# Kernel tuning notes

Measured on AMD Instinct MI355X. Metric: run time of the kernel, lower is better.

## Reference

```python
import jax, jax.numpy as jnp
import numpy as np

N, L, CS, CZ, CH, H = 1, 768, 384, 128, 32, 12
EPS = 1e-5


def _layernorm(x, w, b):
    m = jnp.mean(x, axis=-1, keepdims=True)
    v = jnp.mean((x - m) ** 2, axis=-1, keepdims=True)
    return (x - m) * jax.lax.rsqrt(v + EPS) * w + b


def setup_inputs() -> dict:
    key = jax.random.key(0)
    ks = jax.random.split(key, 12)
    scale = 0.02
    return {
        "s": jax.random.normal(ks[0], (N, L, CS), jnp.float32),
        "z": jax.random.normal(ks[1], (N, L, L, CZ), jnp.float32),
        "ln_s_w": jnp.ones((CS,), jnp.float32),
        "ln_s_b": jnp.zeros((CS,), jnp.float32),
        "ln_z_w": jnp.ones((CZ,), jnp.float32),
        "ln_z_b": jnp.zeros((CZ,), jnp.float32),
        "w_z": jax.random.normal(ks[2], (H, CZ), jnp.float32) * scale,   # pair-bias proj (no bias)
        "w_q": jax.random.normal(ks[3], (H * CH, CS), jnp.float32) * scale,
        "w_k": jax.random.normal(ks[4], (H * CH, CS), jnp.float32) * scale,
        "w_v": jax.random.normal(ks[5], (H * CH, CS), jnp.float32) * scale,
        "w_g": jax.random.normal(ks[6], (H * CH, CS), jnp.float32) * scale,
        "b_g": jnp.zeros((H * CH,), jnp.float32),
        "w_o": jax.random.normal(ks[7], (CS, H * CH), jnp.float32) * scale,
        "b_o": jnp.zeros((CS,), jnp.float32),
    }


def reference(s, z, ln_s_w, ln_s_b, ln_z_w, ln_z_b, w_z, w_q, w_k, w_v, w_g, b_g, w_o, b_o):
    s_n = _layernorm(s, ln_s_w, ln_s_b)            # [N,L,CS]
    z_n = _layernorm(z, ln_z_w, ln_z_b)            # [N,L,L,CZ]
    # pair bias: Linear(c_z -> H, bias=False), then permute to [N,H,L,L]
    bias = jnp.einsum("nijc,hc->nhij", z_n, w_z)   # [N,H,L,L]
    # AF2-style gated MHA on s
    q = jnp.einsum("nlc,dc->nld", s_n, w_q).reshape(N, L, H, CH) * (CH ** -0.5)
    k = jnp.einsum("nlc,dc->nld", s_n, w_k).reshape(N, L, H, CH)
    v = jnp.einsum("nlc,dc->nld", s_n, w_v).reshape(N, L, H, CH)
    logits = jnp.einsum("nqhc,nkhc->nhqk", q, k) + bias
    a = jax.nn.softmax(logits, axis=-1)
    o = jnp.einsum("nhqk,nkhc->nqhc", a, v).reshape(N, L, H * CH)
    g = jax.nn.sigmoid(jnp.einsum("nlc,dc->nld", s_n, w_g) + b_g)
    o = o * g
    return jnp.einsum("nld,cd->nlc", o, w_o) + b_o  # [N,L,CS]
```

## Files before the change

kernel.cpp:

```cpp
#include <hip/hip_runtime.h>
#include <hip/hip_bf16.h>
#include <cstddef>

#define L_ 768
#define CS_ 384
#define CZ_ 128
#define CH_ 32
#define H_ 12
#define LL_ (L_*L_)
#define EPS_ 1e-5f

typedef float f4 __attribute__((ext_vector_type(4)));

__global__ void prep_kernel(const float* __restrict__ lnzw, const float* __restrict__ lnzb,
                            const float* __restrict__ wz,
                            float* __restrict__ ww, float* __restrict__ sumww,
                            float* __restrict__ bb) {
    int h = threadIdx.x;
    if (h < H_) {
        float sw = 0.f, sb = 0.f;
        for (int c = 0; c < CZ_; ++c) {
            float wv = lnzw[c] * wz[h*CZ_ + c];
            ww[h*CZ_ + c] = wv;
            sw += wv;
            sb += lnzb[c] * wz[h*CZ_ + c];
        }
        sumww[h] = sw;
        bb[h] = sb;
    }
}

__device__ __forceinline__ void bias_issue(const float* gbase, float* ldst, int c) {
    #pragma unroll
    for (int j = 0; j < 8; ++j)
        __builtin_amdgcn_global_load_lds(
            (const __attribute__((address_space(1))) unsigned int*)(gbase + c*32 + j*4),
            (__attribute__((address_space(3))) unsigned int*)(ldst + j*1024),
            16, 0, 0);
}

__global__ __launch_bounds__(256) void bias_kernel(const float* __restrict__ z,
        const float* __restrict__ ww, const float* __restrict__ sumww,
        const float* __restrict__ bb, float* __restrict__ bias) {
    __shared__ float zbuf[2*8192];
    __shared__ float lw[H_*CZ_];
    __shared__ float lsw[H_];
    __shared__ float lbb[H_];

    const int tid   = threadIdx.x;
    const int w     = tid >> 6;
    const int l     = tid & 63;
    const int rbase = blockIdx.x * 256;

    const float* gbase = z + (size_t)(rbase + w*64 + l)*CZ_;

    for (int i = tid; i < H_*CZ_; i += 256) lw[i] = ww[i];
    if (tid < H_) { lsw[tid] = sumww[tid]; lbb[tid] = bb[tid]; }

    float acc[H_];
    #pragma unroll
    for (int h = 0; h < H_; ++h) acc[h] = 0.f;
    float sum = 0.f, sum2 = 0.f;

    bias_issue(gbase, zbuf + w*256, 0);
    __syncthreads();

    int cur = 0;
    #pragma unroll 1
    for (int c0 = 0; c0 < 4; ++c0) {
        if (c0 < 3)
            bias_issue(gbase, zbuf + (cur^1)*8192 + w*256, c0+1);
        #pragma unroll
        for (int j = 0; j < 8; ++j) {
            f4 zv = *(const f4*)&zbuf[cur*8192 + j*1024 + tid*4];
            const int cbase = c0*32 + j*4;
            sum  += zv.x + zv.y + zv.z + zv.w;
            sum2 += zv.x*zv.x + zv.y*zv.y + zv.z*zv.z + zv.w*zv.w;
            #pragma unroll
            for (int h = 0; h < H_; ++h) {
                f4 wv = *(const f4*)&lw[h*CZ_ + cbase];
                acc[h] += zv.x*wv.x + zv.y*wv.y + zv.z*wv.z + zv.w*wv.w;
            }
        }
        __syncthreads();
        cur ^= 1;
    }

    float m = sum * (1.f/CZ_);
    float r = rsqrtf(sum2*(1.f/CZ_) - m*m + EPS_);
    #pragma unroll
    for (int h = 0; h < H_; ++h)
        zbuf[tid*17 + h] = r*(acc[h] - m*lsw[h]) + lbb[h];
    __syncthreads();
    #pragma unroll
    for (int it = 0; it < 3; ++it) {
        int idx = it*256 + tid;
        int h   = idx >> 6;
        int qd  = idx & 63;
        f4 o;
        o.x = zbuf[(qd*4 + 0)*17 + h];
        o.y = zbuf[(qd*4 + 1)*17 + h];
        o.z = zbuf[(qd*4 + 2)*17 + h];
        o.w = zbuf[(qd*4 + 3)*17 + h];
        *(f4*)(bias + (size_t)h*LL_ + rbase + qd*4) = o;
    }
}

__global__ void sln_kernel(const float* __restrict__ s, const float* __restrict__ w,
                           const float* __restrict__ b, float* __restrict__ sn) {
    int row = blockIdx.x;
    int lane = threadIdx.x;
    float x[6];
    float sum = 0.f, sum2 = 0.f;
    #pragma unroll
    for (int j = 0; j < 6; ++j) {
        x[j] = s[row*CS_ + lane + j*64];
        sum += x[j]; sum2 += x[j]*x[j];
    }
    #pragma unroll
    for (int off = 32; off; off >>= 1) {
        sum  += __shfl_xor(sum,  off);
        sum2 += __shfl_xor(sum2, off);
    }
    float m = sum * (1.f/CS_);
    float r = rsqrtf(sum2*(1.f/CS_) - m*m + EPS_);
    #pragma unroll
    for (int j = 0; j < 6; ++j) {
        int c = lane + j*64;
        sn[row*CS_ + c] = (x[j]-m)*r*w[c] + b[c];
    }
}

__global__ __launch_bounds__(256) void qkvg_kernel(const float* __restrict__ sn,
        const float* __restrict__ wq, const float* __restrict__ wk,
        const float* __restrict__ wv, const float* __restrict__ wg,
        const float* __restrict__ bg,
        float* __restrict__ qb, float* __restrict__ kb,
        float* __restrict__ vb, float* __restrict__ gb) {
    __shared__ float As[16][68];
    __shared__ float Bs[16][68];
    int m0 = blockIdx.x * 64;
    int n0 = blockIdx.y * 64;
    int sel = n0 / 384;
    const float* W = (sel==0) ? wq : (sel==1) ? wk : (sel==2) ? wv : wg;
    float* C       = (sel==0) ? qb : (sel==1) ? kb : (sel==2) ? vb : gb;
    int ncol0 = n0 - sel*384;

    int t  = threadIdx.x;
    int lr = t >> 2;
    int lc = (t & 3) * 4;
    int ty = t >> 4;
    int tx = t & 15;

    float acc[4][4] = {};
    for (int k0 = 0; k0 < CS_; k0 += 16) {
        float4 av = *(const float4*)(sn + (size_t)(m0 + lr)*CS_ + k0 + lc);
        float4 bv = *(const float4*)(W  + (size_t)(ncol0 + lr)*CS_ + k0 + lc);
        As[lc+0][lr] = av.x; As[lc+1][lr] = av.y; As[lc+2][lr] = av.z; As[lc+3][lr] = av.w;
        Bs[lc+0][lr] = bv.x; Bs[lc+1][lr] = bv.y; Bs[lc+2][lr] = bv.z; Bs[lc+3][lr] = bv.w;
        __syncthreads();
        #pragma unroll
        for (int kk = 0; kk < 16; ++kk) {
            float4 a4 = *(const float4*)&As[kk][ty*4];
            float4 b4 = *(const float4*)&Bs[kk][tx*4];
            float a[4] = {a4.x,a4.y,a4.z,a4.w};
            float bb_[4] = {b4.x,b4.y,b4.z,b4.w};
            #pragma unroll
            for (int i = 0; i < 4; ++i)
                #pragma unroll
                for (int j = 0; j < 4; ++j)
                    acc[i][j] += a[i]*bb_[j];
        }
        __syncthreads();
    }
    #pragma unroll
    for (int i = 0; i < 4; ++i) {
        int row = m0 + ty*4 + i;
        #pragma unroll
        for (int j = 0; j < 4; ++j) {
            int col = ncol0 + tx*4 + j;
            float v = acc[i][j];
            if (sel == 0) v *= 0.17677669529663687f;
            if (sel == 3) v = 1.f/(1.f + __expf(-(v + bg[col])));
            C[(size_t)row*CS_ + col] = v;
        }
    }
}

#define QT_ 8
__global__ __launch_bounds__(256) void attn_kernel(const float* __restrict__ qb,
        const float* __restrict__ kb, const float* __restrict__ vb,
        const float* __restrict__ gb, const float* __restrict__ bias,
        float* __restrict__ og) {
    __shared__ float Sm[QT_][772];
    __shared__ float KVt[CH_][136];
    int h  = blockIdx.x;
    int q0 = blockIdx.y * QT_;
    int t  = threadIdx.x;

    int tq = t >> 5;
    int tk = t & 31;

    float qreg[CH_];
    {
        const float4* qsrc = (const float4*)(qb + (size_t)(q0 + tq)*CS_ + h*CH_);
        #pragma unroll
        for (int i = 0; i < 8; ++i) {
            float4 qv = qsrc[i];
            qreg[i*4+0]=qv.x; qreg[i*4+1]=qv.y; qreg[i*4+2]=qv.z; qreg[i*4+3]=qv.w;
        }
    }

    for (int kt = 0; kt < L_; kt += 128) {
        #pragma unroll
        for (int r2 = 0; r2 < 4; ++r2) {
            int row = (t >> 3) + 32*r2;
            int c   = (t & 7) * 4;
            f4 kv = *(const f4*)(kb + (size_t)(kt+row)*CS_ + h*CH_ + c);
            KVt[c+0][row]=kv.x; KVt[c+1][row]=kv.y; KVt[c+2][row]=kv.z; KVt[c+3][row]=kv.w;
        }
        __syncthreads();
        f4 sacc = {0,0,0,0};
        #pragma unroll
        for (int c = 0; c < CH_; ++c) {
            f4 kv4 = *(const f4*)&KVt[c][tk*4];
            sacc.x += qreg[c]*kv4.x;
            sacc.y += qreg[c]*kv4.y;
            sacc.z += qreg[c]*kv4.z;
            sacc.w += qreg[c]*kv4.w;
        }
        f4 bv = *(const f4*)(bias + (size_t)h*LL_ + (size_t)(q0+tq)*L_ + kt + tk*4);
        *(f4*)&Sm[tq][kt + tk*4] = sacc + bv;
        __syncthreads();
    }

    {
        float mx = -1e30f;
        for (int k = tk; k < L_; k += 32) mx = fmaxf(mx, Sm[tq][k]);
        #pragma unroll
        for (int off = 16; off; off >>= 1) mx = fmaxf(mx, __shfl_xor(mx, off));
        float ssum = 0.f;
        for (int k = tk; k < L_; k += 32) {
            float e = __expf(Sm[tq][k] - mx);
            Sm[tq][k] = e;
            ssum += e;
        }
        #pragma unroll
        for (int off = 16; off; off >>= 1) ssum += __shfl_xor(ssum, off);
        float inv = 1.f/ssum;
        for (int k = tk; k < L_; k += 32) Sm[tq][k] *= inv;
        __syncthreads();
    }

    {
        float o = 0.f;
        for (int kt = 0; kt < L_; kt += 128) {
            #pragma unroll
            for (int r2 = 0; r2 < 4; ++r2) {
                int row = (t >> 3) + 32*r2;
                int c   = (t & 7) * 4;
                f4 vv = *(const f4*)(vb + (size_t)(kt+row)*CS_ + h*CH_ + c);
                KVt[c+0][row]=vv.x; KVt[c+1][row]=vv.y; KVt[c+2][row]=vv.z; KVt[c+3][row]=vv.w;
            }
            __syncthreads();
            #pragma unroll
            for (int j4 = 0; j4 < 32; ++j4) {
                f4 pv = *(const f4*)&Sm[tq][kt + j4*4];
                f4 va = *(const f4*)&KVt[tk][j4*4];
                o += pv.x*va.x + pv.y*va.y + pv.z*va.z + pv.w*va.w;
            }
            __syncthreads();
        }
        int row = q0 + tq;
        int c   = h*CH_ + tk;
        og[(size_t)row*CS_ + c] = o * gb[(size_t)row*CS_ + c];
    }
}

__global__ __launch_bounds__(256) void outproj_kernel(const float* __restrict__ og,
        const float* __restrict__ wo, const float* __restrict__ bo,
        float* __restrict__ out) {
    __shared__ float As[16][68];
    __shared__ float Bs[16][68];
    int m0 = blockIdx.x * 64;
    int n0 = blockIdx.y * 64;
    int t  = threadIdx.x;
    int lr = t >> 2;
    int lc = (t & 3) * 4;
    int ty = t >> 4;
    int tx = t & 15;
    float acc[4][4] = {};
    for (int k0 = 0; k0 < CS_; k0 += 16) {
        float4 av = *(const float4*)(og + (size_t)(m0 + lr)*CS_ + k0 + lc);
        float4 bv = *(const float4*)(wo + (size_t)(n0 + lr)*CS_ + k0 + lc);
        As[lc+0][lr] = av.x; As[lc+1][lr] = av.y; As[lc+2][lr] = av.z; As[lc+3][lr] = av.w;
        Bs[lc+0][lr] = bv.x; Bs[lc+1][lr] = bv.y; Bs[lc+2][lr] = bv.z; Bs[lc+3][lr] = bv.w;
        __syncthreads();
        #pragma unroll
        for (int kk = 0; kk < 16; ++kk) {
            float4 a4 = *(const float4*)&As[kk][ty*4];
            float4 b4 = *(const float4*)&Bs[kk][tx*4];
            float a[4] = {a4.x,a4.y,a4.z,a4.w};
            float bb_[4] = {b4.x,b4.y,b4.z,b4.w};
            #pragma unroll
            for (int i = 0; i < 4; ++i)
                #pragma unroll
                for (int j = 0; j < 4; ++j)
                    acc[i][j] += a[i]*bb_[j];
        }
        __syncthreads();
    }
    #pragma unroll
    for (int i = 0; i < 4; ++i) {
        int row = m0 + ty*4 + i;
        #pragma unroll
        for (int j = 0; j < 4; ++j) {
            int col = n0 + tx*4 + j;
            out[(size_t)row*CS_ + col] = acc[i][j] + bo[col];
        }
    }
}

extern "C" void kernel_launch(void* const* d_in, const int* in_sizes, int n_in,
                              void* d_out, int out_size, void* d_ws, size_t ws_size,
                              hipStream_t stream) {
    const float* s      = (const float*)d_in[0];
    const float* z      = (const float*)d_in[1];
    const float* ln_s_w = (const float*)d_in[2];
    const float* ln_s_b = (const float*)d_in[3];
    const float* ln_z_w = (const float*)d_in[4];
    const float* ln_z_b = (const float*)d_in[5];
    const float* w_z    = (const float*)d_in[6];
    const float* w_q    = (const float*)d_in[7];
    const float* w_k    = (const float*)d_in[8];
    const float* w_v    = (const float*)d_in[9];
    const float* w_g    = (const float*)d_in[10];
    const float* b_g    = (const float*)d_in[11];
    const float* w_o    = (const float*)d_in[12];
    const float* b_o    = (const float*)d_in[13];
    float* out = (float*)d_out;

    float* ws    = (float*)d_ws;
    float* bias  = ws;
    float* sn    = bias + (size_t)H_*LL_;
    float* qb    = sn + (size_t)L_*CS_;
    float* kb    = qb + (size_t)L_*CS_;
    float* vb    = kb + (size_t)L_*CS_;
    float* gb    = vb + (size_t)L_*CS_;
    float* og    = gb + (size_t)L_*CS_;
    float* ww    = og + (size_t)L_*CS_;
    float* sumww = ww + (size_t)H_*CZ_;
    float* bbuf  = sumww + 16;

    hipLaunchKernelGGL(prep_kernel, dim3(1), dim3(64), 0, stream,
                       ln_z_w, ln_z_b, w_z, ww, sumww, bbuf);
    hipLaunchKernelGGL(bias_kernel, dim3(LL_/256), dim3(256), 0, stream,
                       z, ww, sumww, bbuf, bias);
    hipLaunchKernelGGL(sln_kernel, dim3(L_), dim3(64), 0, stream,
                       s, ln_s_w, ln_s_b, sn);
    hipLaunchKernelGGL(qkvg_kernel, dim3(L_/64, 1536/64), dim3(256), 0, stream,
                       sn, w_q, w_k, w_v, w_g, b_g, qb, kb, vb, gb);
    hipLaunchKernelGGL(attn_kernel, dim3(H_, L_/QT_), dim3(256), 0, stream,
                       qb, kb, vb, gb, bias, og);
    hipLaunchKernelGGL(outproj_kernel, dim3(L_/64, CS_/64), dim3(256), 0, stream,
                       og, w_o, b_o, out);
}
```

Measured before the change: 233.2 us.

## Restructure pair-bias kernel with register-staged coalesced loads and two rows per thread

Replaces the direct global-to-LDS async loads in the bias kernel with coalesced nontemporal f4 loads staged through registers, written into a padded LDS tile. Each of 128 threads now handles two z rows, so every weight read from LDS is reused twice. The output transpose through LDS is dropped in favour of direct per-head stores. The aim is better coalescing of the z stream (about 300MB) and less LDS weight traffic, at the cost of higher register pressure (16 staged f4 plus 24 accumulators) and possibly lower occupancy.

```diff
diff --git a/kernel.cpp b/kernel.cpp
--- a/kernel.cpp
+++ b/kernel.cpp
@@ -30,79 +30,78 @@
     }
 }
 
-__device__ __forceinline__ void bias_issue(const float* gbase, float* ldst, int c) {
-    #pragma unroll
-    for (int j = 0; j < 8; ++j)
-        __builtin_amdgcn_global_load_lds(
-            (const __attribute__((address_space(1))) unsigned int*)(gbase + c*32 + j*4),
-            (__attribute__((address_space(3))) unsigned int*)(ldst + j*1024),
-            16, 0, 0);
-}
-
-__global__ __launch_bounds__(256) void bias_kernel(const float* __restrict__ z,
+__global__ __launch_bounds__(128) void bias_kernel(const float* __restrict__ z,
         const float* __restrict__ ww, const float* __restrict__ sumww,
         const float* __restrict__ bb, float* __restrict__ bias) {
-    __shared__ float zbuf[2*8192];
+    __shared__ float zb[2][256][36];
     __shared__ float lw[H_*CZ_];
     __shared__ float lsw[H_];
     __shared__ float lbb[H_];
 
-    const int tid   = threadIdx.x;
-    const int w     = tid >> 6;
-    const int l     = tid & 63;
-    const int rbase = blockIdx.x * 256;
-
-    const float* gbase = z + (size_t)(rbase + w*64 + l)*CZ_;
-
-    for (int i = tid; i < H_*CZ_; i += 256) lw[i] = ww[i];
-    if (tid < H_) { lsw[tid] = sumww[tid]; lbb[tid] = bb[tid]; }
-
-    float acc[H_];
-    #pragma unroll
-    for (int h = 0; h < H_; ++h) acc[h] = 0.f;
-    float sum = 0.f, sum2 = 0.f;
-
-    bias_issue(gbase, zbuf + w*256, 0);
-    __syncthreads();
-
-    int cur = 0;
+    const int t  = threadIdx.x;
+    const size_t tb = (size_t)blockIdx.x * 256;
+    const int sr = t >> 3;
+    const int s8 = t & 7;
+
+    const f4* zf4 = (const f4*)z;
+
+    f4 st[16];
+    #pragma unroll
+    for (int p = 0; p < 16; ++p)
+        st[p] = __builtin_nontemporal_load(&zf4[(tb + p*16 + sr)*32 + s8]);
+
+    {
+        const f4* wwf4 = (const f4*)ww;
+        f4* lwf4 = (f4*)lw;
+        #pragma unroll
+        for (int i = 0; i < 3; ++i) lwf4[i*128 + t] = wwf4[i*128 + t];
+        if (t < H_) { lsw[t] = sumww[t]; lbb[t] = bb[t]; }
+    }
+
+    float acc0[H_], acc1[H_];
+    #pragma unroll
+    for (int h = 0; h < H_; ++h) { acc0[h] = 0.f; acc1[h] = 0.f; }
+    float s0 = 0.f, q0 = 0.f, s1 = 0.f, q1 = 0.f;
+
     #pragma unroll 1
-    for (int c0 = 0; c0 < 4; ++c0) {
-        if (c0 < 3)
-            bias_issue(gbase, zbuf + (cur^1)*8192 + w*256, c0+1);
+    for (int c = 0; c < 4; ++c) {
+        #pragma unroll
+        for (int p = 0; p < 16; ++p)
+            *(f4*)&zb[c&1][p*16 + sr][s8*4] = st[p];
+        if (c < 3) {
+            #pragma unroll
+            for (int p = 0; p < 16; ++p)
+                st[p] = __builtin_nontemporal_load(&zf4[(tb + p*16 + sr)*32 + (c+1)*8 + s8]);
+        }
+        __syncthreads();
+
         #pragma unroll
         for (int j = 0; j < 8; ++j) {
-            f4 zv = *(const f4*)&zbuf[cur*8192 + j*1024 + tid*4];
-            const int cbase = c0*32 + j*4;
-            sum  += zv.x + zv.y + zv.z + zv.w;
-            sum2 += zv.x*zv.x + zv.y*zv.y + zv.z*zv.z + zv.w*zv.w;
+            f4 z0 = *(const f4*)&zb[c&1][t][j*4];
+            f4 z1 = *(const f4*)&zb[c&1][t+128][j*4];
+            s0 += z0.x+z0.y+z0.z+z0.w;
+            q0 += z0.x*z0.x+z0.y*z0.y+z0.z*z0.z+z0.w*z0.w;
+            s1 += z1.x+z1.y+z1.z+z1.w;
+            q1 += z1.x*z1.x+z1.y*z1.y+z1.z*z1.z+z1.w*z1.w;
+            const int cb = c*32 + j*4;
             #pragma unroll
             for (int h = 0; h < H_; ++h) {
-                f4 wv = *(const f4*)&lw[h*CZ_ + cbase];
-                acc[h] += zv.x*wv.x + zv.y*wv.y + zv.z*wv.z + zv.w*wv.w;
+                f4 wv = *(const f4*)&lw[h*CZ_ + cb];
+                acc0[h] += z0.x*wv.x + z0.y*wv.y + z0.z*wv.z + z0.w*wv.w;
+                acc1[h] += z1.x*wv.x + z1.y*wv.y + z1.z*wv.z + z1.w*wv.w;
             }
         }
         __syncthreads();
-        cur ^= 1;
-    }
-
-    float m = sum * (1.f/CZ_);
-    float r = rsqrtf(sum2*(1.f/CZ_) - m*m + EPS_);
-    #pragma unroll
-    for (int h = 0; h < H_; ++h)
-        zbuf[tid*17 + h] = r*(acc[h] - m*lsw[h]) + lbb[h];
-    __syncthreads();
-    #pragma unroll
-    for (int it = 0; it < 3; ++it) {
-        int idx = it*256 + tid;
-        int h   = idx >> 6;
-        int qd  = idx & 63;
-        f4 o;
-        o.x = zbuf[(qd*4 + 0)*17 + h];
-        o.y = zbuf[(qd*4 + 1)*17 + h];
-        o.z = zbuf[(qd*4 + 2)*17 + h];
-        o.w = zbuf[(qd*4 + 3)*17 + h];
-        *(f4*)(bias + (size_t)h*LL_ + rbase + qd*4) = o;
+    }
+
+    float m0 = s0 * (1.f/CZ_);
+    float r0 = rsqrtf(q0*(1.f/CZ_) - m0*m0 + EPS_);
+    float m1 = s1 * (1.f/CZ_);
+    float r1 = rsqrtf(q1*(1.f/CZ_) - m1*m1 + EPS_);
+    #pragma unroll
+    for (int h = 0; h < H_; ++h) {
+        bias[(size_t)h*LL_ + tb + t]       = r0*(acc0[h] - m0*lsw[h]) + lbb[h];
+        bias[(size_t)h*LL_ + tb + 128 + t] = r1*(acc1[h] - m1*lsw[h]) + lbb[h];
     }
 }
 
@@ -354,7 +353,7 @@
 
     hipLaunchKernelGGL(prep_kernel, dim3(1), dim3(64), 0, stream,
                        ln_z_w, ln_z_b, w_z, ww, sumww, bbuf);
-    hipLaunchKernelGGL(bias_kernel, dim3(LL_/256), dim3(256), 0, stream,
+    hipLaunchKernelGGL(bias_kernel, dim3(LL_/256), dim3(128), 0, stream,
                        z, ww, sumww, bbuf, bias);
     hipLaunchKernelGGL(sln_kernel, dim3(L_), dim3(64), 0, stream,
                        s, ln_s_w, ln_s_b, sn);
```

Result: faster. 209.9 us (-10.0%).
